# Kernel optimization log

Hardware: AMD Instinct MI355X
Metric: run time of the kernel (lower is better)

Reference implementation:

```python
import jax, jax.numpy as jnp
import numpy as np

EPS = 1e-5

def rms_norm(x, scale, eps=EPS):
    rms = jax.lax.rsqrt(jnp.mean(x * x, axis=-1, keepdims=True) + eps)
    return scale * (x * rms)

def act_quant(x, min_scale=0.001, max_scale=1000.0):
    # int8 activation quantization (STE in torch; fwd math only here)
    max_val = jnp.max(jnp.abs(x), axis=-1, keepdims=True)
    s = jnp.clip(127.0 / (max_val + 1e-5), min_scale, max_scale)
    return jnp.clip(jnp.round(s * x), -128.0, 127.0) / s

def weight_quant(w, num_bits=8):
    qmax = 2.0 ** (num_bits - 1) - 1.0
    scale = qmax / (jnp.max(jnp.abs(w)) + 1e-5)
    return jnp.round(jnp.clip(w * scale, -(qmax + 1.0), qmax)) / scale

def ternarize(w):
    sf = jnp.clip(1.0 / (jnp.mean(jnp.abs(w)) + 1e-5), 1e-4, 1e4)
    return jnp.sign(w * sf)

def setup_inputs() -> dict:
    key = jax.random.key(0)
    ks = jax.random.split(key, 5)
    B, S, E, H = 8, 512, 2048, 2048
    x = jax.random.normal(ks[0], (B, S, E), dtype=jnp.float32)
    # ternary {-1,0,1} init as in ternary_initialize
    def tern_init(k, shape):
        r = jax.random.uniform(k, shape, dtype=jnp.float32)
        return jnp.where(r < 1.0 / 3.0, -1.0, jnp.where(r > 2.0 / 3.0, 1.0, 0.0))
    return {
        "x": x,
        "rms_scale": jnp.ones((H,), jnp.float32),
        "W_f": tern_init(ks[1], (E, H)),
        "W_c": tern_init(ks[2], (E, H)),
        "W_g": tern_init(ks[3], (H, E)),
        "b_f": jnp.ones((H,), jnp.float32),
        "b_c": jnp.zeros((H,), jnp.float32),
        "b_g": jnp.zeros((H,), jnp.float32),
    }

def reference(x, rms_scale, W_f, W_c, W_g, b_f, b_c, b_g):
    B, S, E = x.shape
    H = W_f.shape[1]
    # quantize + ternarize weights once (identical every timestep)
    Wt_f = ternarize(weight_quant(W_f))
    Wt_c = ternarize(weight_quant(W_c))
    Wt_g = ternarize(weight_quant(W_g))  # (H, E) but E == H

    def step(h, x_t):
        xq = act_quant(rms_norm(x_t, rms_scale))
        # matmul-free linear: x @ (pos_mask - neg_mask) == x @ sign(W)
        f_t = jax.nn.sigmoid(xq @ Wt_f + b_f)
        c_t = jax.nn.silu(xq @ Wt_c + b_c)
        g_t = jax.nn.sigmoid(xq @ Wt_g + b_g)
        h_new = f_t * h + (1.0 - f_t) * c_t
        o_t = g_t * h_new
        # layer-level copy gate: sigmoid(W_g @ x_t^T)^T = sigmoid(x_t @ W_g^T), raw weights
        cg = jax.nn.sigmoid(x_t @ W_g.T)
        h_out = cg * x_t + (1.0 - cg) * h_new
        return h_out, o_t

    h0 = jnp.zeros((B, H), x.dtype)
    _, outs = jax.lax.scan(step, h0, jnp.swapaxes(x, 0, 1))  # scan over S
    return jnp.swapaxes(outs, 0, 1)  # (B, S, H)
```

## Files before the change

### kernel.cpp

```cpp
#include <hip/hip_runtime.h>
#include <hip/hip_bf16.h>
#include <cstdint>
#include <cstddef>

#define RTOT 4096
#define DIM  2048
#define NCAT 6144
#define NCHUNK 16
#define TCHUNK 32

typedef __attribute__((ext_vector_type(4))) int int4v;

__device__ __forceinline__ float fast_sigmoid(float z) {
    return __builtin_amdgcn_rcpf(1.0f + __expf(-z));
}
__device__ __forceinline__ unsigned short f2h(float f) {
    union { _Float16 h; unsigned short u; } v; v.h = (_Float16)f; return v.u;
}
__device__ __forceinline__ float h2f(unsigned short u) {
    union { _Float16 h; unsigned short u; } v; v.u = u; return (float)v.h;
}

#define GLDS(gp, lp) __builtin_amdgcn_global_load_lds( \
    (__attribute__((address_space(1))) const void*)(gp), \
    (__attribute__((address_space(3))) void*)(lp), 16, 0, 0)

__device__ __forceinline__ int4v frag_ld(const signed char* lds, int R, int lq) {
    return *(const int4v*)(lds + R * 64 + ((lq ^ ((R >> 1) & 3)) * 16));
}

__global__ __launch_bounds__(256) void prep_all(
    const float* __restrict__ x, const float* __restrict__ scale,
    const float* __restrict__ Wf, const float* __restrict__ Wc,
    const float* __restrict__ Wg,
    signed char* __restrict__ WcatT, signed char* __restrict__ Wgb,
    signed char* __restrict__ Xq, signed char* __restrict__ Q1,
    signed char* __restrict__ Q2, float* __restrict__ s_arr,
    float* __restrict__ s1_arr)
{
    __shared__ __align__(16) char smem[4224];
    int bid = blockIdx.x;
    int tid = threadIdx.x;
    if (bid < 3072) {
        signed char (*tile)[65] = (signed char(*)[65])smem;
        int j0 = (bid % 96) * 64;
        int k0 = (bid / 96) * 64;
        const float* W = (j0 < 2048) ? Wf : (j0 < 4096) ? Wc : Wg;
        int jb = j0 & 2047;
        int c  = tid & 63;
        int rr = tid >> 6;
#pragma unroll
        for (int p = 0; p < 16; ++p) {
            int kl = p * 4 + rr;
            tile[kl][c] = (signed char)(int)W[(size_t)(k0 + kl) * DIM + jb + c];
        }
        __syncthreads();
#pragma unroll
        for (int p = 0; p < 16; ++p) {
            int jl = p * 4 + rr;
            WcatT[(size_t)(j0 + jl) * DIM + k0 + c] = tile[c][jl];
        }
    } else if (bid < 4096) {
        int idx = (bid - 3072) * 4096 + tid * 16;
#pragma unroll
        for (int p = 0; p < 4; ++p) {
            float4 v = *(const float4*)(Wg + idx + p * 4);
            char4 o;
            o.x = (signed char)(int)v.x; o.y = (signed char)(int)v.y;
            o.z = (signed char)(int)v.z; o.w = (signed char)(int)v.w;
            *(char4*)(Wgb + idx + p * 4) = o;
        }
    } else {
        float* red = (float*)smem;
        float* tot = (float*)(smem + 64);
        int row = bid - 4096;
        const float* xr = x + (size_t)row * DIM + tid * 8;
        const float* sr = scale + tid * 8;
        float4 a0 = *(const float4*)(xr);
        float4 a1 = *(const float4*)(xr + 4);
        float4 c0 = *(const float4*)(sr);
        float4 c1 = *(const float4*)(sr + 4);
        float xs[8] = {a0.x, a0.y, a0.z, a0.w, a1.x, a1.y, a1.z, a1.w};
        float sc[8] = {c0.x, c0.y, c0.z, c0.w, c1.x, c1.y, c1.z, c1.w};
        float sum = 0.f, mx2 = 0.f;
#pragma unroll
        for (int i = 0; i < 8; ++i) {
            sum += xs[i] * xs[i];
            mx2 = fmaxf(mx2, fabsf(xs[i]));
        }
#pragma unroll
        for (int off = 32; off > 0; off >>= 1) {
            sum += __shfl_down(sum, off);
            mx2 = fmaxf(mx2, __shfl_down(mx2, off));
        }
        int lane = tid & 63, wv = tid >> 6;
        if (lane == 0) { red[wv] = sum; red[4 + wv] = mx2; }
        __syncthreads();
        if (tid == 0) {
            tot[0] = red[0] + red[1] + red[2] + red[3];
            tot[1] = fmaxf(fmaxf(red[4], red[5]), fmaxf(red[6], red[7]));
        }
        __syncthreads();
        float rms = 1.0f / sqrtf(tot[0] * (1.0f / 2048.0f) + 1e-5f);
        float y[8]; float mx = 0.f;
#pragma unroll
        for (int i = 0; i < 8; ++i) {
            y[i] = (xs[i] * rms) * sc[i];
            mx = fmaxf(mx, fabsf(y[i]));
        }
#pragma unroll
        for (int off = 32; off > 0; off >>= 1) mx = fmaxf(mx, __shfl_down(mx, off));
        if (lane == 0) red[8 + wv] = mx;
        __syncthreads();
        if (tid == 0)
            tot[2] = fmaxf(fmaxf(red[8], red[9]), fmaxf(red[10], red[11]));
        __syncthreads();
        float s = 127.0f / (tot[2] + 1e-5f);
        s = fminf(fmaxf(s, 0.001f), 1000.0f);
        float s1 = 127.0f / (tot[1] + 1e-5f);
        float inv_s1 = 1.0f / s1;
        if (tid == 0) { s_arr[row] = s; s1_arr[row] = s1; }
        signed char q8[8], q1b[8], q2b[8];
#pragma unroll
        for (int i = 0; i < 8; ++i) {
            float q = fminf(fmaxf(rintf(s * y[i]), -128.f), 127.f);
            q8[i] = (signed char)(int)q;
            float qq1 = fminf(fmaxf(rintf(s1 * xs[i]), -128.f), 127.f);
            q1b[i] = (signed char)(int)qq1;
            float r = xs[i] - qq1 * inv_s1;
            float qq2 = fminf(fmaxf(rintf(s1 * 256.f * r), -128.f), 127.f);
            q2b[i] = (signed char)(int)qq2;
        }
        size_t o = (size_t)row * DIM + tid * 8;
        *(int2*)(Xq + o) = *(int2*)q8;
        *(int2*)(Q1 + o) = *(int2*)q1b;
        *(int2*)(Q2 + o) = *(int2*)q2b;
    }
}

__global__ __launch_bounds__(256) void gemm_all(
    const signed char* __restrict__ Xq, const signed char* __restrict__ WcatT,
    const signed char* __restrict__ Q1, const signed char* __restrict__ Q2,
    const signed char* __restrict__ Wgb,
    const float* __restrict__ s_arr, const float* __restrict__ s1_arr,
    const float* __restrict__ b_f, const float* __restrict__ b_c,
    const float* __restrict__ b_g,
    unsigned short* __restrict__ FCG,
    unsigned short* __restrict__ U,
    unsigned short* __restrict__ V)
{
    __shared__ __align__(16) signed char lds[32768];
    int bid = blockIdx.x;
    int grp = bid / 5, r5 = bid % 5;
    int tid = threadIdx.x;
    int lane = tid & 63, wv = tid >> 6;
    int lr = lane & 15, lq = lane >> 4;
    int rA = lane >> 2;
    int gch = ((lane & 3) ^ ((lane >> 3) & 3)) * 16;

    if (r5 < 3) {
        int fb = grp * 3 + r5;
        int m0 = (fb / 48) * 128;
        int n0 = (fb % 48) * 128;
        int wm = (wv >> 1) * 64, wn = (wv & 1) * 64;
        const signed char* Ab = Xq + (size_t)m0 * DIM;
        const signed char* Bb = WcatT + (size_t)n0 * DIM;

        int4v acc[4][4] = {};
#pragma unroll
        for (int it = 0; it < 2; ++it) {
            int region = wv + it * 4;
            int rr = region * 16 + rA;
            GLDS(Ab + (size_t)rr * DIM + gch, lds + region * 1024);
            GLDS(Bb + (size_t)rr * DIM + gch, lds + 8192 + region * 1024);
        }
        for (int k6 = 0; k6 < 32; ++k6) {
            signed char* cur = lds + (k6 & 1) * 16384;
            signed char* nxt = lds + ((k6 + 1) & 1) * 16384;
            __syncthreads();
            if (k6 + 1 < 32) {
                int kt = (k6 + 1) * 64;
#pragma unroll
                for (int it = 0; it < 2; ++it) {
                    int region = wv + it * 4;
                    int rr = region * 16 + rA;
                    GLDS(Ab + (size_t)rr * DIM + kt + gch, nxt + region * 1024);
                    GLDS(Bb + (size_t)rr * DIM + kt + gch, nxt + 8192 + region * 1024);
                }
            }
            int4v af[4], bb[4];
#pragma unroll
            for (int i = 0; i < 4; ++i) af[i] = frag_ld(cur, wm + i * 16 + lr, lq);
#pragma unroll
            for (int j = 0; j < 4; ++j) bb[j] = frag_ld(cur + 8192, wn + j * 16 + lr, lq);
#pragma unroll
            for (int i = 0; i < 4; ++i)
#pragma unroll
                for (int j = 0; j < 4; ++j)
                    acc[i][j] = __builtin_amdgcn_mfma_i32_16x16x64_i8(
                        af[i], bb[j], acc[i][j], 0, 0, 0);
        }
#pragma unroll
        for (int i = 0; i < 4; ++i) {
            float rinv[4];
#pragma unroll
            for (int r = 0; r < 4; ++r)
                rinv[r] = __builtin_amdgcn_rcpf(s_arr[m0 + wm + i * 16 + lq * 4 + r]);
#pragma unroll
            for (int j = 0; j < 4; ++j) {
                int gcol = n0 + wn + j * 16 + lr;
                int sec = gcol >> 11;
                int jj = gcol & 2047;
                float bias = (sec == 0) ? b_f[jj] : (sec == 1) ? b_c[jj] : b_g[jj];
#pragma unroll
                for (int r = 0; r < 4; ++r) {
                    int grow = m0 + wm + i * 16 + lq * 4 + r;
                    float z = fmaf((float)acc[i][j][r], rinv[r], bias);
                    float sg = fast_sigmoid(z);
                    FCG[(size_t)grow * NCAT + gcol] = f2h((sec == 1) ? z * sg : sg);
                }
            }
        }
    } else {
        int cb = grp * 2 + (r5 - 3);
        int m0 = (cb >> 4) * 64;
        int n0 = (cb & 15) * 128;
        int wm = (wv >> 1) * 32, wn = (wv & 1) * 64;
        const signed char* A1b = Q1 + (size_t)m0 * DIM;
        const signed char* A2b = Q2 + (size_t)m0 * DIM;
        const signed char* Bb  = Wgb + (size_t)n0 * DIM;
        int r1 = wv * 16 + rA;

        int4v acc1[2][4] = {};
        int4v acc2[2][4] = {};
        {
            GLDS(A1b + (size_t)r1 * DIM + gch, lds + wv * 1024);
            GLDS(A2b + (size_t)r1 * DIM + gch, lds + 4096 + wv * 1024);
#pragma unroll
            for (int it = 0; it < 2; ++it) {
                int region = wv + it * 4;
                int rr = region * 16 + rA;
                GLDS(Bb + (size_t)rr * DIM + gch, lds + 8192 + region * 1024);
            }
        }
        for (int k6 = 0; k6 < 32; ++k6) {
            signed char* cur = lds + (k6 & 1) * 16384;
            signed char* nxt = lds + ((k6 + 1) & 1) * 16384;
            __syncthreads();
            if (k6 + 1 < 32) {
                int kt = (k6 + 1) * 64;
                GLDS(A1b + (size_t)r1 * DIM + kt + gch, nxt + wv * 1024);
                GLDS(A2b + (size_t)r1 * DIM + kt + gch, nxt + 4096 + wv * 1024);
#pragma unroll
                for (int it = 0; it < 2; ++it) {
                    int region = wv + it * 4;
                    int rr = region * 16 + rA;
                    GLDS(Bb + (size_t)rr * DIM + kt + gch, nxt + 8192 + region * 1024);
                }
            }
            int4v bb[4];
#pragma unroll
            for (int j = 0; j < 4; ++j) bb[j] = frag_ld(cur + 8192, wn + j * 16 + lr, lq);
#pragma unroll
            for (int i = 0; i < 2; ++i) {
                int4v a1 = frag_ld(cur, wm + i * 16 + lr, lq);
                int4v a2 = frag_ld(cur + 4096, wm + i * 16 + lr, lq);
#pragma unroll
                for (int j = 0; j < 4; ++j) {
                    acc1[i][j] = __builtin_amdgcn_mfma_i32_16x16x64_i8(
                        a1, bb[j], acc1[i][j], 0, 0, 0);
                    acc2[i][j] = __builtin_amdgcn_mfma_i32_16x16x64_i8(
                        a2, bb[j], acc2[i][j], 0, 0, 0);
                }
            }
        }
#pragma unroll
        for (int i = 0; i < 2; ++i) {
            float rinv[4];
#pragma unroll
            for (int r = 0; r < 4; ++r)
                rinv[r] = __builtin_amdgcn_rcpf(s1_arr[m0 + wm + i * 16 + lq * 4 + r]);
#pragma unroll
            for (int j = 0; j < 4; ++j) {
                int gcol = n0 + wn + j * 16 + lr;
#pragma unroll
                for (int r = 0; r < 4; ++r) {
                    int grow = m0 + wm + i * 16 + lq * 4 + r;
                    size_t go = (size_t)grow * DIM + gcol;
                    float zs = (float)acc1[i][j][r] + (float)acc2[i][j][r] * (1.f / 256.f);
                    float cg = fast_sigmoid(zs * rinv[r]);
                    float xv = ((float)Q1[go] + (float)Q2[go] * (1.f / 256.f)) * rinv[r];
                    U[go] = f2h(cg * xv);
                    V[go] = f2h(1.f - cg);
                }
            }
        }
    }
}

__global__ __launch_bounds__(256) void scan_partial(
    const unsigned short* __restrict__ FCG, const unsigned short* __restrict__ U,
    const unsigned short* __restrict__ V, float4* __restrict__ PQ4)
{
    int tp = blockIdx.x * 256 + threadIdx.x;
    int c = blockIdx.y;
    int b = blockIdx.z;
    int h0 = tp * 2;
    size_t r0 = (size_t)(b * 512 + c * TCHUNK);
    const unsigned short* fp = FCG + r0 * NCAT + h0;
    const unsigned short* up = U + r0 * DIM + h0;
    const unsigned short* vp = V + r0 * DIM + h0;
    float P0 = 1.f, Q0 = 0.f, P1 = 1.f, Q1v = 0.f;
#pragma unroll 4
    for (int t = 0; t < TCHUNK; ++t) {
        unsigned fw = *(const unsigned*)(fp);
        unsigned cw = *(const unsigned*)(fp + 2048);
        unsigned uw = *(const unsigned*)(up);
        unsigned vw = *(const unsigned*)(vp);
        float f0 = h2f(fw & 0xffff), f1 = h2f(fw >> 16);
        float c0 = h2f(cw & 0xffff), c1 = h2f(cw >> 16);
        float u0 = h2f(uw & 0xffff), u1 = h2f(uw >> 16);
        float v0 = h2f(vw & 0xffff), v1 = h2f(vw >> 16);
        float A0 = v0 * f0, A1 = v1 * f1;
        float B0 = fmaf(v0 * (1.f - f0), c0, u0);
        float B1 = fmaf(v1 * (1.f - f1), c1, u1);
        P0 = A0 * P0; Q0 = fmaf(A0, Q0, B0);
        P1 = A1 * P1; Q1v = fmaf(A1, Q1v, B1);
        fp += NCAT; up += DIM; vp += DIM;
    }
    float4 o; o.x = P0; o.y = Q0; o.z = P1; o.w = Q1v;
    PQ4[(size_t)c * 8192 + b * 1024 + tp] = o;
}

__global__ __launch_bounds__(256) void scan_final(
    const unsigned short* __restrict__ FCG, const unsigned short* __restrict__ U,
    const unsigned short* __restrict__ V, const float4* __restrict__ PQ4,
    float* __restrict__ out)
{
    int tp = blockIdx.x * 256 + threadIdx.x;
    int c = blockIdx.y;
    int b = blockIdx.z;
    int h0 = tp * 2;
    float h0s = 0.f, h1s = 0.f;
    for (int cc = 0; cc < c; ++cc) {
        float4 pq = PQ4[(size_t)cc * 8192 + b * 1024 + tp];
        h0s = fmaf(pq.x, h0s, pq.y);
        h1s = fmaf(pq.z, h1s, pq.w);
    }
    size_t r0 = (size_t)(b * 512 + c * TCHUNK);
    const unsigned short* fp = FCG + r0 * NCAT + h0;
    const unsigned short* up = U + r0 * DIM + h0;
    const unsigned short* vp = V + r0 * DIM + h0;
    float* op = out + r0 * DIM + h0;
#pragma unroll 4
    for (int t = 0; t < TCHUNK; ++t) {
        unsigned fw = *(const unsigned*)(fp);
        unsigned cw = *(const unsigned*)(fp + 2048);
        unsigned gw = *(const unsigned*)(fp + 4096);
        unsigned uw = *(const unsigned*)(up);
        unsigned vw = *(const unsigned*)(vp);
        float f0 = h2f(fw & 0xffff), f1 = h2f(fw >> 16);
        float c0 = h2f(cw & 0xffff), c1 = h2f(cw >> 16);
        float g0 = h2f(gw & 0xffff), g1 = h2f(gw >> 16);
        float u0 = h2f(uw & 0xffff), u1 = h2f(uw >> 16);
        float v0 = h2f(vw & 0xffff), v1 = h2f(vw >> 16);
        float hn0 = f0 * h0s + (1.f - f0) * c0;
        float hn1 = f1 * h1s + (1.f - f1) * c1;
        float2 ov; ov.x = g0 * hn0; ov.y = g1 * hn1;
        *(float2*)op = ov;
        h0s = fmaf(v0, hn0, u0);
        h1s = fmaf(v1, hn1, u1);
        fp += NCAT; up += DIM; vp += DIM; op += DIM;
    }
}

extern "C" void kernel_launch(void* const* d_in, const int* in_sizes, int n_in,
                              void* d_out, int out_size, void* d_ws, size_t ws_size,
                              hipStream_t stream) {
    const float* x     = (const float*)d_in[0];
    const float* rmssc = (const float*)d_in[1];
    const float* W_f   = (const float*)d_in[2];
    const float* W_c   = (const float*)d_in[3];
    const float* W_g   = (const float*)d_in[4];
    const float* b_f   = (const float*)d_in[5];
    const float* b_c   = (const float*)d_in[6];
    const float* b_g   = (const float*)d_in[7];
    float* out = (float*)d_out;

    char* ws = (char*)d_ws;
    size_t off = 0;
    auto alloc = [&](size_t bytes) -> void* {
        void* p = ws + off;
        off += (bytes + 255) & ~(size_t)255;
        return p;
    };
    signed char* WcatT = (signed char*)alloc((size_t)NCAT * DIM);
    signed char* Wgb   = (signed char*)alloc((size_t)DIM * DIM);
    signed char* Xq    = (signed char*)alloc((size_t)RTOT * DIM);
    signed char* Q1    = (signed char*)alloc((size_t)RTOT * DIM);
    signed char* Q2    = (signed char*)alloc((size_t)RTOT * DIM);
    float* s_arr       = (float*)alloc((size_t)RTOT * 4);
    float* s1_arr      = (float*)alloc((size_t)RTOT * 4);
    unsigned short* FCG = (unsigned short*)alloc((size_t)RTOT * NCAT * 2);
    unsigned short* U   = (unsigned short*)alloc((size_t)RTOT * DIM * 2);
    unsigned short* V   = (unsigned short*)alloc((size_t)RTOT * DIM * 2);
    float4* PQ4        = (float4*)alloc((size_t)NCHUNK * 8192 * 16);

    hipLaunchKernelGGL(prep_all, dim3(8192), dim3(256), 0, stream,
                       x, rmssc, W_f, W_c, W_g, WcatT, Wgb, Xq, Q1, Q2,
                       s_arr, s1_arr);
    hipLaunchKernelGGL(gemm_all, dim3(2560), dim3(256), 0, stream,
                       Xq, WcatT, Q1, Q2, Wgb, s_arr, s1_arr,
                       b_f, b_c, b_g, FCG, U, V);
    hipLaunchKernelGGL(scan_partial, dim3(DIM / 512, NCHUNK, 8), dim3(256), 0, stream,
                       FCG, U, V, PQ4);
    hipLaunchKernelGGL(scan_final, dim3(DIM / 512, NCHUNK, 8), dim3(256), 0, stream,
                       FCG, U, V, PQ4, out);
}
```

Baseline: 297.3 us.

## Switch GEMMs to 32x32x32 int8 MFMA with wider N tiles; halve scan chunk length

```diff
diff --git a/kernel.cpp b/kernel.cpp
--- a/kernel.cpp
+++ b/kernel.cpp
@@ -6,10 +6,11 @@
 #define RTOT 4096
 #define DIM  2048
 #define NCAT 6144
-#define NCHUNK 16
-#define TCHUNK 32
-
-typedef __attribute__((ext_vector_type(4))) int int4v;
+#define NCHUNK 32
+#define TCHUNK 16
+
+typedef __attribute__((ext_vector_type(4)))  int int4v;
+typedef __attribute__((ext_vector_type(16))) int int16v;
 
 __device__ __forceinline__ float fast_sigmoid(float z) {
     return __builtin_amdgcn_rcpf(1.0f + __expf(-z));
@@ -25,8 +26,9 @@
     (__attribute__((address_space(1))) const void*)(gp), \
     (__attribute__((address_space(3))) void*)(lp), 16, 0, 0)
 
-__device__ __forceinline__ int4v frag_ld(const signed char* lds, int R, int lq) {
-    return *(const int4v*)(lds + R * 64 + ((lq ^ ((R >> 1) & 3)) * 16));
+__device__ __forceinline__ int4v frag32(const signed char* lds, int R, int ks,
+                                        int h5) {
+    return *(const int4v*)(lds + R * 64 + (((ks * 2 + h5) ^ ((R >> 1) & 3)) * 16));
 }
 
 __global__ __launch_bounds__(256) void prep_all(
@@ -149,73 +151,82 @@
     unsigned short* __restrict__ U,
     unsigned short* __restrict__ V)
 {
-    __shared__ __align__(16) signed char lds[32768];
+    __shared__ __align__(16) signed char lds[49152];
     int bid = blockIdx.x;
     int grp = bid / 5, r5 = bid % 5;
     int tid = threadIdx.x;
     int lane = tid & 63, wv = tid >> 6;
-    int lr = lane & 15, lq = lane >> 4;
+    int l31 = lane & 31, h5 = lane >> 5;
     int rA = lane >> 2;
     int gch = ((lane & 3) ^ ((lane >> 3) & 3)) * 16;
 
     if (r5 < 3) {
         int fb = grp * 3 + r5;
-        int m0 = (fb / 48) * 128;
-        int n0 = (fb % 48) * 128;
-        int wm = (wv >> 1) * 64, wn = (wv & 1) * 64;
+        int m0 = (fb / 24) * 128;
+        int n0 = (fb % 24) * 256;
+        int wm = (wv >> 1) * 64, wn = (wv & 1) * 128;
         const signed char* Ab = Xq + (size_t)m0 * DIM;
         const signed char* Bb = WcatT + (size_t)n0 * DIM;
 
-        int4v acc[4][4] = {};
-#pragma unroll
-        for (int it = 0; it < 2; ++it) {
+        int16v acc[2][4] = {};
+#pragma unroll
+        for (int it = 0; it < 6; ++it) {
             int region = wv + it * 4;
-            int rr = region * 16 + rA;
-            GLDS(Ab + (size_t)rr * DIM + gch, lds + region * 1024);
-            GLDS(Bb + (size_t)rr * DIM + gch, lds + 8192 + region * 1024);
+            const signed char* g = (region < 8)
+                ? Ab + (size_t)(region * 16 + rA) * DIM
+                : Bb + (size_t)((region - 8) * 16 + rA) * DIM;
+            GLDS(g + gch, lds + region * 1024);
         }
         for (int k6 = 0; k6 < 32; ++k6) {
-            signed char* cur = lds + (k6 & 1) * 16384;
-            signed char* nxt = lds + ((k6 + 1) & 1) * 16384;
+            const signed char* cur = lds + (k6 & 1) * 24576;
+            signed char* nxt = lds + ((k6 + 1) & 1) * 24576;
             __syncthreads();
             if (k6 + 1 < 32) {
                 int kt = (k6 + 1) * 64;
 #pragma unroll
-                for (int it = 0; it < 2; ++it) {
+                for (int it = 0; it < 6; ++it) {
                     int region = wv + it * 4;
-                    int rr = region * 16 + rA;
-                    GLDS(Ab + (size_t)rr * DIM + kt + gch, nxt + region * 1024);
-                    GLDS(Bb + (size_t)rr * DIM + kt + gch, nxt + 8192 + region * 1024);
+                    const signed char* g = (region < 8)
+                        ? Ab + (size_t)(region * 16 + rA) * DIM
+                        : Bb + (size_t)((region - 8) * 16 + rA) * DIM;
+                    GLDS(g + kt + gch, nxt + region * 1024);
                 }
             }
-            int4v af[4], bb[4];
-#pragma unroll
-            for (int i = 0; i < 4; ++i) af[i] = frag_ld(cur, wm + i * 16 + lr, lq);
-#pragma unroll
-            for (int j = 0; j < 4; ++j) bb[j] = frag_ld(cur + 8192, wn + j * 16 + lr, lq);
-#pragma unroll
-            for (int i = 0; i < 4; ++i)
-#pragma unroll
-                for (int j = 0; j < 4; ++j)
-                    acc[i][j] = __builtin_amdgcn_mfma_i32_16x16x64_i8(
-                        af[i], bb[j], acc[i][j], 0, 0, 0);
-        }
-#pragma unroll
-        for (int i = 0; i < 4; ++i) {
-            float rinv[4];
-#pragma unroll
-            for (int r = 0; r < 4; ++r)
-                rinv[r] = __builtin_amdgcn_rcpf(s_arr[m0 + wm + i * 16 + lq * 4 + r]);
-#pragma unroll
-            for (int j = 0; j < 4; ++j) {
-                int gcol = n0 + wn + j * 16 + lr;
+#pragma unroll
+            for (int ks = 0; ks < 2; ++ks) {
+                int4v af[2], bb[4];
+#pragma unroll
+                for (int mi = 0; mi < 2; ++mi)
+                    af[mi] = frag32(cur, wm + mi * 32 + l31, ks, h5);
+#pragma unroll
+                for (int nj = 0; nj < 4; ++nj)
+                    bb[nj] = frag32(cur + 8192, wn + nj * 32 + l31, ks, h5);
+#pragma unroll
+                for (int mi = 0; mi < 2; ++mi)
+#pragma unroll
+                    for (int nj = 0; nj < 4; ++nj)
+                        acc[mi][nj] = __builtin_amdgcn_mfma_i32_32x32x32_i8(
+                            af[mi], bb[nj], acc[mi][nj], 0, 0, 0);
+            }
+        }
+#pragma unroll
+        for (int mi = 0; mi < 2; ++mi) {
+            float rinv[16];
+#pragma unroll
+            for (int r = 0; r < 16; ++r) {
+                int grow = m0 + wm + mi * 32 + (r & 3) + 8 * (r >> 2) + 4 * h5;
+                rinv[r] = __builtin_amdgcn_rcpf(s_arr[grow]);
+            }
+#pragma unroll
+            for (int nj = 0; nj < 4; ++nj) {
+                int gcol = n0 + wn + nj * 32 + l31;
                 int sec = gcol >> 11;
                 int jj = gcol & 2047;
                 float bias = (sec == 0) ? b_f[jj] : (sec == 1) ? b_c[jj] : b_g[jj];
 #pragma unroll
-                for (int r = 0; r < 4; ++r) {
-                    int grow = m0 + wm + i * 16 + lq * 4 + r;
-                    float z = fmaf((float)acc[i][j][r], rinv[r], bias);
+                for (int r = 0; r < 16; ++r) {
+                    int grow = m0 + wm + mi * 32 + (r & 3) + 8 * (r >> 2) + 4 * h5;
+                    float z = fmaf((float)acc[mi][nj][r], rinv[r], bias);
                     float sg = fast_sigmoid(z);
                     FCG[(size_t)grow * NCAT + gcol] = f2h((sec == 1) ? z * sg : sg);
                 }
@@ -223,76 +234,77 @@
         }
     } else {
         int cb = grp * 2 + (r5 - 3);
-        int m0 = (cb >> 4) * 64;
-        int n0 = (cb & 15) * 128;
-        int wm = (wv >> 1) * 32, wn = (wv & 1) * 64;
+        int m0 = (cb >> 3) * 64;
+        int n0 = (cb & 7) * 256;
+        int wm = (wv >> 1) * 32, wn = (wv & 1) * 128;
         const signed char* A1b = Q1 + (size_t)m0 * DIM;
         const signed char* A2b = Q2 + (size_t)m0 * DIM;
         const signed char* Bb  = Wgb + (size_t)n0 * DIM;
-        int r1 = wv * 16 + rA;
-
-        int4v acc1[2][4] = {};
-        int4v acc2[2][4] = {};
-        {
-            GLDS(A1b + (size_t)r1 * DIM + gch, lds + wv * 1024);
-            GLDS(A2b + (size_t)r1 * DIM + gch, lds + 4096 + wv * 1024);
-#pragma unroll
-            for (int it = 0; it < 2; ++it) {
-                int region = wv + it * 4;
-                int rr = region * 16 + rA;
-                GLDS(Bb + (size_t)rr * DIM + gch, lds + 8192 + region * 1024);
-            }
+
+        int16v acc1[4] = {};
+        int16v acc2[4] = {};
+#pragma unroll
+        for (int it = 0; it < 6; ++it) {
+            int region = wv + it * 4;
+            const signed char* g = (region < 4)
+                ? A1b + (size_t)(region * 16 + rA) * DIM
+                : (region < 8)
+                    ? A2b + (size_t)((region - 4) * 16 + rA) * DIM
+                    : Bb + (size_t)((region - 8) * 16 + rA) * DIM;
+            GLDS(g + gch, lds + region * 1024);
         }
         for (int k6 = 0; k6 < 32; ++k6) {
-            signed char* cur = lds + (k6 & 1) * 16384;
-            signed char* nxt = lds + ((k6 + 1) & 1) * 16384;
+            const signed char* cur = lds + (k6 & 1) * 24576;
+            signed char* nxt = lds + ((k6 + 1) & 1) * 24576;
             __syncthreads();
             if (k6 + 1 < 32) {
                 int kt = (k6 + 1) * 64;
-                GLDS(A1b + (size_t)r1 * DIM + kt + gch, nxt + wv * 1024);
-                GLDS(A2b + (size_t)r1 * DIM + kt + gch, nxt + 4096 + wv * 1024);
-#pragma unroll
-                for (int it = 0; it < 2; ++it) {
+#pragma unroll
+                for (int it = 0; it < 6; ++it) {
                     int region = wv + it * 4;
-                    int rr = region * 16 + rA;
-                    GLDS(Bb + (size_t)rr * DIM + kt + gch, nxt + 8192 + region * 1024);
+                    const signed char* g = (region < 4)
+                        ? A1b + (size_t)(region * 16 + rA) * DIM
+                        : (region < 8)
+                            ? A2b + (size_t)((region - 4) * 16 + rA) * DIM
+                            : Bb + (size_t)((region - 8) * 16 + rA) * DIM;
+                    GLDS(g + kt + gch, nxt + region * 1024);
                 }
             }
-            int4v bb[4];
-#pragma unroll
-            for (int j = 0; j < 4; ++j) bb[j] = frag_ld(cur + 8192, wn + j * 16 + lr, lq);
-#pragma unroll
-            for (int i = 0; i < 2; ++i) {
-                int4v a1 = frag_ld(cur, wm + i * 16 + lr, lq);
-                int4v a2 = frag_ld(cur + 4096, wm + i * 16 + lr, lq);
-#pragma unroll
-                for (int j = 0; j < 4; ++j) {
-                    acc1[i][j] = __builtin_amdgcn_mfma_i32_16x16x64_i8(
-                        a1, bb[j], acc1[i][j], 0, 0, 0);
-                    acc2[i][j] = __builtin_amdgcn_mfma_i32_16x16x64_i8(
-                        a2, bb[j], acc2[i][j], 0, 0, 0);
+#pragma unroll
+            for (int ks = 0; ks < 2; ++ks) {
+                int4v a1 = frag32(cur, wm + l31, ks, h5);
+                int4v a2 = frag32(cur + 4096, wm + l31, ks, h5);
+                int4v bb[4];
+#pragma unroll
+                for (int nj = 0; nj < 4; ++nj)
+                    bb[nj] = frag32(cur + 8192, wn + nj * 32 + l31, ks, h5);
+#pragma unroll
+                for (int nj = 0; nj < 4; ++nj) {
+                    acc1[nj] = __builtin_amdgcn_mfma_i32_32x32x32_i8(
+                        a1, bb[nj], acc1[nj], 0, 0, 0);
+                    acc2[nj] = __builtin_amdgcn_mfma_i32_32x32x32_i8(
+                        a2, bb[nj], acc2[nj], 0, 0, 0);
                 }
             }
         }
-#pragma unroll
-        for (int i = 0; i < 2; ++i) {
-            float rinv[4];
-#pragma unroll
-            for (int r = 0; r < 4; ++r)
-                rinv[r] = __builtin_amdgcn_rcpf(s1_arr[m0 + wm + i * 16 + lq * 4 + r]);
-#pragma unroll
-            for (int j = 0; j < 4; ++j) {
-                int gcol = n0 + wn + j * 16 + lr;
-#pragma unroll
-                for (int r = 0; r < 4; ++r) {
-                    int grow = m0 + wm + i * 16 + lq * 4 + r;
-                    size_t go = (size_t)grow * DIM + gcol;
-                    float zs = (float)acc1[i][j][r] + (float)acc2[i][j][r] * (1.f / 256.f);
-                    float cg = fast_sigmoid(zs * rinv[r]);
-                    float xv = ((float)Q1[go] + (float)Q2[go] * (1.f / 256.f)) * rinv[r];
-                    U[go] = f2h(cg * xv);
-                    V[go] = f2h(1.f - cg);
-                }
+        float rinv[16];
+#pragma unroll
+        for (int r = 0; r < 16; ++r) {
+            int grow = m0 + wm + (r & 3) + 8 * (r >> 2) + 4 * h5;
+            rinv[r] = __builtin_amdgcn_rcpf(s1_arr[grow]);
+        }
+#pragma unroll
+        for (int nj = 0; nj < 4; ++nj) {
+            int gcol = n0 + wn + nj * 32 + l31;
+#pragma unroll
+            for (int r = 0; r < 16; ++r) {
+                int grow = m0 + wm + (r & 3) + 8 * (r >> 2) + 4 * h5;
+                size_t go = (size_t)grow * DIM + gcol;
+                float zs = (float)acc1[nj][r] + (float)acc2[nj][r] * (1.f / 256.f);
+                float cg = fast_sigmoid(zs * rinv[r]);
+                float xv = ((float)Q1[go] + (float)Q2[go] * (1.f / 256.f)) * rinv[r];
+                U[go] = f2h(cg * xv);
+                V[go] = f2h(1.f - cg);
             }
         }
     }
@@ -409,11 +421,11 @@
     hipLaunchKernelGGL(prep_all, dim3(8192), dim3(256), 0, stream,
                        x, rmssc, W_f, W_c, W_g, WcatT, Wgb, Xq, Q1, Q2,
                        s_arr, s1_arr);
-    hipLaunchKernelGGL(gemm_all, dim3(2560), dim3(256), 0, stream,
+    hipLaunchKernelGGL(gemm_all, dim3(1280), dim3(256), 0, stream,
                        Xq, WcatT, Q1, Q2, Wgb, s_arr, s1_arr,
                        b_f, b_c, b_g, FCG, U, V);
-    hipLaunchKernelGGL(scan_partial, dim3(DIM / 512, NCHUNK, 8), dim3(256), 0, stream,
+    hipLaunchKernelGGL(scan_partial, dim3(4, NCHUNK, 8), dim3(256), 0, stream,
                        FCG, U, V, PQ4);
-    hipLaunchKernelGGL(scan_final, dim3(DIM / 512, NCHUNK, 8), dim3(256), 0, stream,
+    hipLaunchKernelGGL(scan_final, dim3(4, NCHUNK, 8), dim3(256), 0, stream,
                        FCG, U, V, PQ4, out);
 }
```

New measurement: 298.4 us. Within noise of the previous version (+0.4%).

## Pre-pack GEMM operands into MFMA fragment layout and load directly to registers

Applied to the files above, without the earlier changes.

```diff
diff --git a/kernel.cpp b/kernel.cpp
--- a/kernel.cpp
+++ b/kernel.cpp
@@ -6,8 +6,10 @@
 #define RTOT 4096
 #define DIM  2048
 #define NCAT 6144
-#define NCHUNK 16
-#define TCHUNK 32
+#define NCHUNK 32
+#define TCHUNK 16
+#define FRAG  1024
+#define KT    32
 
 typedef __attribute__((ext_vector_type(4))) int int4v;
 
@@ -19,24 +21,16 @@
 }
 __device__ __forceinline__ float h2f(unsigned short u) {
     union { _Float16 h; unsigned short u; } v; v.u = u; return (float)v.h;
-}
-
-#define GLDS(gp, lp) __builtin_amdgcn_global_load_lds( \
-    (__attribute__((address_space(1))) const void*)(gp), \
-    (__attribute__((address_space(3))) void*)(lp), 16, 0, 0)
-
-__device__ __forceinline__ int4v frag_ld(const signed char* lds, int R, int lq) {
-    return *(const int4v*)(lds + R * 64 + ((lq ^ ((R >> 1) & 3)) * 16));
 }
 
 __global__ __launch_bounds__(256) void prep_all(
     const float* __restrict__ x, const float* __restrict__ scale,
     const float* __restrict__ Wf, const float* __restrict__ Wc,
     const float* __restrict__ Wg,
-    signed char* __restrict__ WcatT, signed char* __restrict__ Wgb,
-    signed char* __restrict__ Xq, signed char* __restrict__ Q1,
-    signed char* __restrict__ Q2, float* __restrict__ s_arr,
-    float* __restrict__ s1_arr)
+    signed char* __restrict__ PWcat, signed char* __restrict__ PWg,
+    signed char* __restrict__ PXq, signed char* __restrict__ PQ1,
+    signed char* __restrict__ PQ2, unsigned short* __restrict__ Xh,
+    float* __restrict__ s_arr, float* __restrict__ s1_arr)
 {
     __shared__ __align__(16) char smem[4224];
     int bid = blockIdx.x;
@@ -55,21 +49,29 @@
             tile[kl][c] = (signed char)(int)W[(size_t)(k0 + kl) * DIM + jb + c];
         }
         __syncthreads();
-#pragma unroll
-        for (int p = 0; p < 16; ++p) {
-            int jl = p * 4 + rr;
-            WcatT[(size_t)(j0 + jl) * DIM + k0 + c] = tile[c][jl];
-        }
+        int f = tid >> 6, l = tid & 63;
+        int lr = l & 15, lq = l >> 4;
+        signed char frag[16];
+#pragma unroll
+        for (int b = 0; b < 16; ++b) frag[b] = tile[lq * 16 + b][f * 16 + lr];
+        signed char* dst = PWcat +
+            ((size_t)((j0 >> 4) + f) * KT + (k0 >> 6)) * FRAG + l * 16;
+        *(int4v*)dst = *(int4v*)frag;
     } else if (bid < 4096) {
-        int idx = (bid - 3072) * 4096 + tid * 16;
+        int fid = (bid - 3072) * 4 + (tid >> 6);
+        int nt = fid >> 5, kt = fid & 31;
+        int l = tid & 63, lr = l & 15, lq = l >> 4;
+        const float* src = Wg + (size_t)(nt * 16 + lr) * DIM + kt * 64 + lq * 16;
+        signed char frag[16];
 #pragma unroll
         for (int p = 0; p < 4; ++p) {
-            float4 v = *(const float4*)(Wg + idx + p * 4);
-            char4 o;
-            o.x = (signed char)(int)v.x; o.y = (signed char)(int)v.y;
-            o.z = (signed char)(int)v.z; o.w = (signed char)(int)v.w;
-            *(char4*)(Wgb + idx + p * 4) = o;
-        }
+            float4 v = *(const float4*)(src + p * 4);
+            frag[p * 4 + 0] = (signed char)(int)v.x;
+            frag[p * 4 + 1] = (signed char)(int)v.y;
+            frag[p * 4 + 2] = (signed char)(int)v.z;
+            frag[p * 4 + 3] = (signed char)(int)v.w;
+        }
+        *(int4v*)(PWg + (size_t)fid * FRAG + l * 16) = *(int4v*)frag;
     } else {
         float* red = (float*)smem;
         float* tot = (float*)(smem + 64);
@@ -121,6 +123,7 @@
         float inv_s1 = 1.0f / s1;
         if (tid == 0) { s_arr[row] = s; s1_arr[row] = s1; }
         signed char q8[8], q1b[8], q2b[8];
+        unsigned short hx[8];
 #pragma unroll
         for (int i = 0; i < 8; ++i) {
             float q = fminf(fmaxf(rintf(s * y[i]), -128.f), 127.f);
@@ -130,91 +133,87 @@
             float r = xs[i] - qq1 * inv_s1;
             float qq2 = fminf(fmaxf(rintf(s1 * 256.f * r), -128.f), 127.f);
             q2b[i] = (signed char)(int)qq2;
-        }
-        size_t o = (size_t)row * DIM + tid * 8;
-        *(int2*)(Xq + o) = *(int2*)q8;
-        *(int2*)(Q1 + o) = *(int2*)q1b;
-        *(int2*)(Q2 + o) = *(int2*)q2b;
+            hx[i] = f2h(xs[i]);
+        }
+        size_t off = ((size_t)(row >> 4) * KT + (tid >> 3)) * FRAG
+                   + ((tid >> 1) & 3) * 256 + (row & 15) * 16 + (tid & 1) * 8;
+        *(int2*)(PXq + off) = *(int2*)q8;
+        *(int2*)(PQ1 + off) = *(int2*)q1b;
+        *(int2*)(PQ2 + off) = *(int2*)q2b;
+        *(int4v*)(Xh + (size_t)row * DIM + tid * 8) = *(int4v*)hx;
     }
 }
 
 __global__ __launch_bounds__(256) void gemm_all(
-    const signed char* __restrict__ Xq, const signed char* __restrict__ WcatT,
-    const signed char* __restrict__ Q1, const signed char* __restrict__ Q2,
-    const signed char* __restrict__ Wgb,
+    const signed char* __restrict__ PXq, const signed char* __restrict__ PWcat,
+    const signed char* __restrict__ PQ1, const signed char* __restrict__ PQ2,
+    const signed char* __restrict__ PWg, const unsigned short* __restrict__ Xh,
     const float* __restrict__ s_arr, const float* __restrict__ s1_arr,
     const float* __restrict__ b_f, const float* __restrict__ b_c,
     const float* __restrict__ b_g,
-    unsigned short* __restrict__ FCG,
-    unsigned short* __restrict__ U,
+    unsigned short* __restrict__ FCG, unsigned short* __restrict__ U,
     unsigned short* __restrict__ V)
 {
-    __shared__ __align__(16) signed char lds[32768];
     int bid = blockIdx.x;
     int grp = bid / 5, r5 = bid % 5;
     int tid = threadIdx.x;
     int lane = tid & 63, wv = tid >> 6;
     int lr = lane & 15, lq = lane >> 4;
-    int rA = lane >> 2;
-    int gch = ((lane & 3) ^ ((lane >> 3) & 3)) * 16;
 
     if (r5 < 3) {
-        int fb = grp * 3 + r5;
-        int m0 = (fb / 48) * 128;
-        int n0 = (fb % 48) * 128;
-        int wm = (wv >> 1) * 64, wn = (wv & 1) * 64;
-        const signed char* Ab = Xq + (size_t)m0 * DIM;
-        const signed char* Bb = WcatT + (size_t)n0 * DIM;
+        int wt = (grp * 3 + r5) * 4 + wv;
+        int m64 = wt / 96, n64 = wt % 96;
+        int m0 = m64 * 64, n0 = n64 * 64;
+        const signed char* Ab = PXq + (size_t)(m64 * 4) * (KT * FRAG) + lane * 16;
+        const signed char* Bb = PWcat + (size_t)(n64 * 4) * (KT * FRAG) + lane * 16;
 
         int4v acc[4][4] = {};
-#pragma unroll
-        for (int it = 0; it < 2; ++it) {
-            int region = wv + it * 4;
-            int rr = region * 16 + rA;
-            GLDS(Ab + (size_t)rr * DIM + gch, lds + region * 1024);
-            GLDS(Bb + (size_t)rr * DIM + gch, lds + 8192 + region * 1024);
-        }
-        for (int k6 = 0; k6 < 32; ++k6) {
-            signed char* cur = lds + (k6 & 1) * 16384;
-            signed char* nxt = lds + ((k6 + 1) & 1) * 16384;
-            __syncthreads();
-            if (k6 + 1 < 32) {
-                int kt = (k6 + 1) * 64;
-#pragma unroll
-                for (int it = 0; it < 2; ++it) {
-                    int region = wv + it * 4;
-                    int rr = region * 16 + rA;
-                    GLDS(Ab + (size_t)rr * DIM + kt + gch, nxt + region * 1024);
-                    GLDS(Bb + (size_t)rr * DIM + kt + gch, nxt + 8192 + region * 1024);
-                }
-            }
-            int4v af[4], bb[4];
-#pragma unroll
-            for (int i = 0; i < 4; ++i) af[i] = frag_ld(cur, wm + i * 16 + lr, lq);
-#pragma unroll
-            for (int j = 0; j < 4; ++j) bb[j] = frag_ld(cur + 8192, wn + j * 16 + lr, lq);
+        int4v a0[4], b0[4], a1[4], b1[4];
+#pragma unroll
+        for (int i = 0; i < 4; ++i) {
+            a0[i] = *(const int4v*)(Ab + i * (KT * FRAG));
+            b0[i] = *(const int4v*)(Bb + i * (KT * FRAG));
+        }
+        for (int kt = 0; kt < KT; kt += 2) {
+#pragma unroll
+            for (int i = 0; i < 4; ++i) {
+                a1[i] = *(const int4v*)(Ab + i * (KT * FRAG) + (kt + 1) * FRAG);
+                b1[i] = *(const int4v*)(Bb + i * (KT * FRAG) + (kt + 1) * FRAG);
+            }
 #pragma unroll
             for (int i = 0; i < 4; ++i)
 #pragma unroll
                 for (int j = 0; j < 4; ++j)
                     acc[i][j] = __builtin_amdgcn_mfma_i32_16x16x64_i8(
-                        af[i], bb[j], acc[i][j], 0, 0, 0);
+                        a0[i], b0[j], acc[i][j], 0, 0, 0);
+            int ktn = (kt + 2) & (KT - 1);
+#pragma unroll
+            for (int i = 0; i < 4; ++i) {
+                a0[i] = *(const int4v*)(Ab + i * (KT * FRAG) + ktn * FRAG);
+                b0[i] = *(const int4v*)(Bb + i * (KT * FRAG) + ktn * FRAG);
+            }
+#pragma unroll
+            for (int i = 0; i < 4; ++i)
+#pragma unroll
+                for (int j = 0; j < 4; ++j)
+                    acc[i][j] = __builtin_amdgcn_mfma_i32_16x16x64_i8(
+                        a1[i], b1[j], acc[i][j], 0, 0, 0);
         }
 #pragma unroll
         for (int i = 0; i < 4; ++i) {
             float rinv[4];
 #pragma unroll
             for (int r = 0; r < 4; ++r)
-                rinv[r] = __builtin_amdgcn_rcpf(s_arr[m0 + wm + i * 16 + lq * 4 + r]);
+                rinv[r] = __builtin_amdgcn_rcpf(s_arr[m0 + i * 16 + lq * 4 + r]);
 #pragma unroll
             for (int j = 0; j < 4; ++j) {
-                int gcol = n0 + wn + j * 16 + lr;
+                int gcol = n0 + j * 16 + lr;
                 int sec = gcol >> 11;
                 int jj = gcol & 2047;
                 float bias = (sec == 0) ? b_f[jj] : (sec == 1) ? b_c[jj] : b_g[jj];
 #pragma unroll
                 for (int r = 0; r < 4; ++r) {
-                    int grow = m0 + wm + i * 16 + lq * 4 + r;
+                    int grow = m0 + i * 16 + lq * 4 + r;
                     float z = fmaf((float)acc[i][j][r], rinv[r], bias);
                     float sg = fast_sigmoid(z);
                     FCG[(size_t)grow * NCAT + gcol] = f2h((sec == 1) ? z * sg : sg);
@@ -222,74 +221,76 @@
             }
         }
     } else {
-        int cb = grp * 2 + (r5 - 3);
-        int m0 = (cb >> 4) * 64;
-        int n0 = (cb & 15) * 128;
-        int wm = (wv >> 1) * 32, wn = (wv & 1) * 64;
-        const signed char* A1b = Q1 + (size_t)m0 * DIM;
-        const signed char* A2b = Q2 + (size_t)m0 * DIM;
-        const signed char* Bb  = Wgb + (size_t)n0 * DIM;
-        int r1 = wv * 16 + rA;
+        int wt = (grp * 2 + (r5 - 3)) * 4 + wv;
+        int m32 = wt >> 5, n64 = wt & 31;
+        int m0 = m32 * 32, n0 = n64 * 64;
+        const signed char* A1b = PQ1 + (size_t)(m32 * 2) * (KT * FRAG) + lane * 16;
+        const signed char* A2b = PQ2 + (size_t)(m32 * 2) * (KT * FRAG) + lane * 16;
+        const signed char* Bb  = PWg + (size_t)(n64 * 4) * (KT * FRAG) + lane * 16;
 
         int4v acc1[2][4] = {};
         int4v acc2[2][4] = {};
-        {
-            GLDS(A1b + (size_t)r1 * DIM + gch, lds + wv * 1024);
-            GLDS(A2b + (size_t)r1 * DIM + gch, lds + 4096 + wv * 1024);
-#pragma unroll
-            for (int it = 0; it < 2; ++it) {
-                int region = wv + it * 4;
-                int rr = region * 16 + rA;
-                GLDS(Bb + (size_t)rr * DIM + gch, lds + 8192 + region * 1024);
-            }
-        }
-        for (int k6 = 0; k6 < 32; ++k6) {
-            signed char* cur = lds + (k6 & 1) * 16384;
-            signed char* nxt = lds + ((k6 + 1) & 1) * 16384;
-            __syncthreads();
-            if (k6 + 1 < 32) {
-                int kt = (k6 + 1) * 64;
-                GLDS(A1b + (size_t)r1 * DIM + kt + gch, nxt + wv * 1024);
-                GLDS(A2b + (size_t)r1 * DIM + kt + gch, nxt + 4096 + wv * 1024);
-#pragma unroll
-                for (int it = 0; it < 2; ++it) {
-                    int region = wv + it * 4;
-                    int rr = region * 16 + rA;
-                    GLDS(Bb + (size_t)rr * DIM + kt + gch, nxt + 8192 + region * 1024);
-                }
-            }
-            int4v bb[4];
-#pragma unroll
-            for (int j = 0; j < 4; ++j) bb[j] = frag_ld(cur + 8192, wn + j * 16 + lr, lq);
+        int4v p0[4], b0[4], p1[4], b1[4];
+#pragma unroll
+        for (int i = 0; i < 2; ++i) {
+            p0[i]     = *(const int4v*)(A1b + i * (KT * FRAG));
+            p0[2 + i] = *(const int4v*)(A2b + i * (KT * FRAG));
+        }
+#pragma unroll
+        for (int j = 0; j < 4; ++j) b0[j] = *(const int4v*)(Bb + j * (KT * FRAG));
+        for (int kt = 0; kt < KT; kt += 2) {
 #pragma unroll
             for (int i = 0; i < 2; ++i) {
-                int4v a1 = frag_ld(cur, wm + i * 16 + lr, lq);
-                int4v a2 = frag_ld(cur + 4096, wm + i * 16 + lr, lq);
+                p1[i]     = *(const int4v*)(A1b + i * (KT * FRAG) + (kt + 1) * FRAG);
+                p1[2 + i] = *(const int4v*)(A2b + i * (KT * FRAG) + (kt + 1) * FRAG);
+            }
+#pragma unroll
+            for (int j = 0; j < 4; ++j)
+                b1[j] = *(const int4v*)(Bb + j * (KT * FRAG) + (kt + 1) * FRAG);
+#pragma unroll
+            for (int i = 0; i < 2; ++i)
 #pragma unroll
                 for (int j = 0; j < 4; ++j) {
                     acc1[i][j] = __builtin_amdgcn_mfma_i32_16x16x64_i8(
-                        a1, bb[j], acc1[i][j], 0, 0, 0);
+                        p0[i], b0[j], acc1[i][j], 0, 0, 0);
                     acc2[i][j] = __builtin_amdgcn_mfma_i32_16x16x64_i8(
-                        a2, bb[j], acc2[i][j], 0, 0, 0);
+                        p0[2 + i], b0[j], acc2[i][j], 0, 0, 0);
                 }
-            }
+            int ktn = (kt + 2) & (KT - 1);
+#pragma unroll
+            for (int i = 0; i < 2; ++i) {
+                p0[i]     = *(const int4v*)(A1b + i * (KT * FRAG) + ktn * FRAG);
+                p0[2 + i] = *(const int4v*)(A2b + i * (KT * FRAG) + ktn * FRAG);
+            }
+#pragma unroll
+            for (int j = 0; j < 4; ++j)
+                b0[j] = *(const int4v*)(Bb + j * (KT * FRAG) + ktn * FRAG);
+#pragma unroll
+            for (int i = 0; i < 2; ++i)
+#pragma unroll
+                for (int j = 0; j < 4; ++j) {
+                    acc1[i][j] = __builtin_amdgcn_mfma_i32_16x16x64_i8(
+                        p1[i], b1[j], acc1[i][j], 0, 0, 0);
+                    acc2[i][j] = __builtin_amdgcn_mfma_i32_16x16x64_i8(
+                        p1[2 + i], b1[j], acc2[i][j], 0, 0, 0);
+                }
         }
 #pragma unroll
         for (int i = 0; i < 2; ++i) {
             float rinv[4];
 #pragma unroll
             for (int r = 0; r < 4; ++r)
-                rinv[r] = __builtin_amdgcn_rcpf(s1_arr[m0 + wm + i * 16 + lq * 4 + r]);
+                rinv[r] = __builtin_amdgcn_rcpf(s1_arr[m0 + i * 16 + lq * 4 + r]);
 #pragma unroll
             for (int j = 0; j < 4; ++j) {
-                int gcol = n0 + wn + j * 16 + lr;
+                int gcol = n0 + j * 16 + lr;
 #pragma unroll
                 for (int r = 0; r < 4; ++r) {
-                    int grow = m0 + wm + i * 16 + lq * 4 + r;
+                    int grow = m0 + i * 16 + lq * 4 + r;
                     size_t go = (size_t)grow * DIM + gcol;
                     float zs = (float)acc1[i][j][r] + (float)acc2[i][j][r] * (1.f / 256.f);
                     float cg = fast_sigmoid(zs * rinv[r]);
-                    float xv = ((float)Q1[go] + (float)Q2[go] * (1.f / 256.f)) * rinv[r];
+                    float xv = h2f(Xh[go]);
                     U[go] = f2h(cg * xv);
                     V[go] = f2h(1.f - cg);
                 }
@@ -394,11 +395,12 @@
         off += (bytes + 255) & ~(size_t)255;
         return p;
     };
-    signed char* WcatT = (signed char*)alloc((size_t)NCAT * DIM);
-    signed char* Wgb   = (signed char*)alloc((size_t)DIM * DIM);
-    signed char* Xq    = (signed char*)alloc((size_t)RTOT * DIM);
-    signed char* Q1    = (signed char*)alloc((size_t)RTOT * DIM);
-    signed char* Q2    = (signed char*)alloc((size_t)RTOT * DIM);
+    signed char* PWcat = (signed char*)alloc((size_t)NCAT * DIM);
+    signed char* PWg   = (signed char*)alloc((size_t)DIM * DIM);
+    signed char* PXq   = (signed char*)alloc((size_t)RTOT * DIM);
+    signed char* PQ1   = (signed char*)alloc((size_t)RTOT * DIM);
+    signed char* PQ2   = (signed char*)alloc((size_t)RTOT * DIM);
+    unsigned short* Xh = (unsigned short*)alloc((size_t)RTOT * DIM * 2);
     float* s_arr       = (float*)alloc((size_t)RTOT * 4);
     float* s1_arr      = (float*)alloc((size_t)RTOT * 4);
     unsigned short* FCG = (unsigned short*)alloc((size_t)RTOT * NCAT * 2);
@@ -407,13 +409,13 @@
     float4* PQ4        = (float4*)alloc((size_t)NCHUNK * 8192 * 16);
 
     hipLaunchKernelGGL(prep_all, dim3(8192), dim3(256), 0, stream,
-                       x, rmssc, W_f, W_c, W_g, WcatT, Wgb, Xq, Q1, Q2,
-                       s_arr, s1_arr);
+                       x, rmssc, W_f, W_c, W_g, PWcat, PWg, PXq, PQ1, PQ2,
+                       Xh, s_arr, s1_arr);
     hipLaunchKernelGGL(gemm_all, dim3(2560), dim3(256), 0, stream,
-                       Xq, WcatT, Q1, Q2, Wgb, s_arr, s1_arr,
+                       PXq, PWcat, PQ1, PQ2, PWg, Xh, s_arr, s1_arr,
                        b_f, b_c, b_g, FCG, U, V);
-    hipLaunchKernelGGL(scan_partial, dim3(DIM / 512, NCHUNK, 8), dim3(256), 0, stream,
+    hipLaunchKernelGGL(scan_partial, dim3(4, NCHUNK, 8), dim3(256), 0, stream,
                        FCG, U, V, PQ4);
-    hipLaunchKernelGGL(scan_final, dim3(DIM / 512, NCHUNK, 8), dim3(256), 0, stream,
+    hipLaunchKernelGGL(scan_final, dim3(4, NCHUNK, 8), dim3(256), 0, stream,
                        FCG, U, V, PQ4, out);
 }
```

Result: slower. 456.5 us (+53.6%).
